# Optimization experiments

Measured on AMD Instinct MI355X. Metric: run time of the kernel, lower is better.

Reference implementation:

```python
import jax, jax.numpy as jnp
import numpy as np

B, T, D, H, FF = 4, 2048, 1024, 16, 4096
HD = D // H
EPS = 1e-5


def layernorm(x, g, b):
    m = jnp.mean(x, axis=-1, keepdims=True)
    v = jnp.var(x, axis=-1, keepdims=True)
    return (x - m) * jax.lax.rsqrt(v + EPS) * g + b


def setup_inputs() -> dict:
    key = jax.random.key(0)
    ks = jax.random.split(key, 12)
    s = lambda fan_in: 1.0 / np.sqrt(fan_in)
    x = jax.random.normal(ks[0], (B, T, D), dtype=jnp.float32)
    mask = jnp.tril(jnp.ones((T, T), dtype=jnp.int32))[None, None]  # [1,1,T,T] causal
    return {
        "x": x,
        "mask": mask,
        "ln1_g": jnp.ones((D,), jnp.float32),
        "ln1_b": jnp.zeros((D,), jnp.float32),
        "ln2_g": jnp.ones((D,), jnp.float32),
        "ln2_b": jnp.zeros((D,), jnp.float32),
        "qkv_w": jax.random.normal(ks[1], (D, 3 * D), jnp.float32) * s(D),
        "out_w": jax.random.normal(ks[2], (D, D), jnp.float32) * s(D),
        "out_b": jnp.zeros((D,), jnp.float32),
        "fc1_w": jax.random.normal(ks[3], (D, FF), jnp.float32) * s(D),
        "fc1_b": jnp.zeros((FF,), jnp.float32),
        "fc2_w": jax.random.normal(ks[4], (FF, D), jnp.float32) * s(FF),
        "fc2_b": jnp.zeros((D,), jnp.float32),
    }


def reference(x, mask, ln1_g, ln1_b, ln2_g, ln2_b, qkv_w, out_w, out_b,
              fc1_w, fc1_b, fc2_w, fc2_b):
    # --- attention sublayer (pre-LN) ---
    h = layernorm(x, ln1_g, ln1_b)
    qkv = h @ qkv_w  # [B,T,3D]
    q, k, v = jnp.split(qkv, 3, axis=-1)
    q = q.reshape(B, T, H, HD).transpose(0, 2, 1, 3)  # [B,H,T,hd]
    k = k.reshape(B, T, H, HD).transpose(0, 2, 1, 3)
    v = v.reshape(B, T, H, HD).transpose(0, 2, 1, 3)
    scale = 1.0 / np.sqrt(HD)
    scores = jnp.einsum('bhqd,bhkd->bhqk', q, k) * scale  # [B,H,T,T]
    scores = jnp.where(mask == 0, -jnp.inf, scores)
    attn = jax.nn.softmax(scores, axis=-1)
    o = jnp.einsum('bhqk,bhkd->bhqd', attn, v)
    o = o.transpose(0, 2, 1, 3).reshape(B, T, D)
    x = x + (o @ out_w + out_b)
    # --- MLP sublayer (pre-LN) ---
    h = layernorm(x, ln2_g, ln2_b)
    h = jax.nn.gelu(h @ fc1_w + fc1_b, approximate=False)
    x = x + (h @ fc2_w + fc2_b)
    return x
```

## Files before the change

### kernel.cpp

```cpp
#include <hip/hip_runtime.h>

typedef unsigned short bfraw;
typedef __attribute__((ext_vector_type(8))) short short8;
typedef __attribute__((ext_vector_type(4))) float f32x4;

__device__ __forceinline__ float b2f(bfraw u){ return __uint_as_float(((unsigned int)u)<<16); }
__device__ __forceinline__ bfraw f2b(float f){
  unsigned int u = __float_as_uint(f);
  return (bfraw)((u + 0x7FFFu + ((u>>16)&1u)) >> 16);
}
__device__ __forceinline__ void store_out(float* p, float v){ *p = v; }
__device__ __forceinline__ void store_out(bfraw* p, float v){ *p = f2b(v); }
__device__ __forceinline__ void gload_lds16(const bfraw* g, short* l) {
  __builtin_amdgcn_global_load_lds((const __attribute__((address_space(1))) void*)g,
                                   (__attribute__((address_space(3))) void*)l, 16, 0, 0);
}
__device__ __forceinline__ unsigned int cvt_pk_bf16(float a, float b) {
  unsigned int r;
  asm("v_cvt_pk_bf16_f32 %0, %1, %2" : "=v"(r) : "v"(a), "v"(b));
  return r;
}
__device__ __forceinline__ void waitvm3(){ asm volatile("s_waitcnt vmcnt(3)" ::: "memory"); }
__device__ __forceinline__ void waitvm0(){ asm volatile("s_waitcnt vmcnt(0)" ::: "memory"); }

__global__ __launch_bounds__(1024) void transpose_f32_bf16(const float* __restrict__ in,
                                                           bfraw* __restrict__ out,
                                                           int R, int C) {
  __shared__ bfraw tile[64][65];
  const int tx = threadIdx.x, ty = threadIdx.y;
  const int c0 = blockIdx.x*64, r0 = blockIdx.y*64;
  #pragma unroll
  for (int u = 0; u < 4; ++u)
    tile[ty + u*16][tx] = f2b(in[(size_t)(r0 + ty + u*16)*C + c0 + tx]);
  __syncthreads();
  #pragma unroll
  for (int u = 0; u < 4; ++u)
    out[(size_t)(c0 + ty + u*16)*R + r0 + tx] = tile[tx][ty + u*16];
}

__global__ __launch_bounds__(256) void ln_kernel(const float* __restrict__ x,
                                                 const float* __restrict__ g,
                                                 const float* __restrict__ b,
                                                 bfraw* __restrict__ out) {
  const int row = blockIdx.x, tid = threadIdx.x;
  const f32x4 v = ((const f32x4*)(x + (size_t)row*1024))[tid];
  float s  = v[0]+v[1]+v[2]+v[3];
  float s2 = v[0]*v[0]+v[1]*v[1]+v[2]*v[2]+v[3]*v[3];
  #pragma unroll
  for (int off = 1; off < 64; off <<= 1) { s += __shfl_xor(s, off); s2 += __shfl_xor(s2, off); }
  __shared__ float red[8];
  const int wv = tid>>6, ln_ = tid&63;
  if (ln_ == 0) { red[wv] = s; red[4+wv] = s2; }
  __syncthreads();
  float a  = red[0]+red[1]+red[2]+red[3];
  float a2 = red[4]+red[5]+red[6]+red[7];
  float mean = a*(1.0f/1024.0f);
  float var  = a2*(1.0f/1024.0f) - mean*mean;
  float inv  = rsqrtf(var + 1e-5f);
  const f32x4 gr = ((const f32x4*)g)[tid];
  const f32x4 br = ((const f32x4*)b)[tid];
  ushort4 o4;
  o4.x = f2b((v[0]-mean)*inv*gr[0] + br[0]);
  o4.y = f2b((v[1]-mean)*inv*gr[1] + br[1]);
  o4.z = f2b((v[2]-mean)*inv*gr[2] + br[2]);
  o4.w = f2b((v[3]-mean)*inv*gr[3] + br[3]);
  ((ushort4*)(out + (size_t)row*1024))[tid] = o4;
}

template<int EPI, typename OutT>
__global__ __launch_bounds__(512, 2) void gemm_bn128(const bfraw* __restrict__ A,
                                                     const bfraw* __restrict__ Bt,
                                                     const float* __restrict__ bias,
                                                     const float* __restrict__ resid,
                                                     OutT* __restrict__ C,
                                                     int M, int N, int K) {
  __shared__ __align__(16) short As[2*2*8192];
  __shared__ __align__(16) short Bs[2*2*4096];
  const int tid = threadIdx.x;
  const int wv = tid>>6, lane = tid&63;
  const int wm = wv>>1, wn = wv&1;
  const int q_ = lane>>4, r = lane&15;
  const int nbm = M>>8, nbn = N>>7;
  const int nwg = nbm*nbn;
  int id = (int)blockIdx.x;
  id = (id&7)*(nwg>>3) + (id>>3);
  const int bm = id % nbm, bn = id / nbm;

  const int srow = tid>>2, sch = tid&3;
  const int sP   = (srow&3) ^ ((srow>>2)&1);
  const int se   = ((sch ^ sP) << 3);
  const bfraw* Ag = A  + (size_t)(bm*256 + srow)*K + se;
  const bfraw* Bg = Bt + (size_t)(bn*128 + srow)*K + se;
  const size_t rowstepA = (size_t)128*K;

  auto stage = [&](int s, int k0s, int nb) {
    const bfraw* ga = Ag + k0s + s*32;
    short* da = As + (nb*2+s)*8192 + tid*8;
    gload_lds16(ga, da);
    gload_lds16(ga + rowstepA, da + 4096);
    const bfraw* gb = Bg + k0s + s*32;
    short* db = Bs + (nb*2+s)*4096 + tid*8;
    gload_lds16(gb, db);
  };

  const int xsw = ((q_ ^ (r&3) ^ ((r>>2)&1)) << 3);
  const int axo = (wm*64 + r)*32 + xsw;
  const int bxo = (wn*64 + r)*32 + xsw;

  f32x4 acc[4][4];
  #pragma unroll
  for (int mi = 0; mi < 4; ++mi)
    #pragma unroll
    for (int ni = 0; ni < 4; ++ni)
      acc[mi][ni] = (f32x4){0.f, 0.f, 0.f, 0.f};

  stage(0, 0, 0); stage(1, 0, 0);
  waitvm3();
  __builtin_amdgcn_s_barrier();

  const int ntiles = K >> 6;
  short8 af[4], bf[4];
  for (int t = 0; t < ntiles; ++t) {
    const int buf = t & 1, nb = buf ^ 1;
    const int k1 = (t + 1) << 6;
    const bool more = (t + 1) < ntiles;

    {
      const short* Ab = As + (buf*2+0)*8192;
      const short* Bb = Bs + (buf*2+0)*4096;
      #pragma unroll
      for (int ni = 0; ni < 4; ++ni) bf[ni] = *(const short8*)&Bb[bxo + ni*512];
      #pragma unroll
      for (int m = 0; m < 4; ++m)   af[m]  = *(const short8*)&Ab[axo + m*512];
    }
    if (more) stage(0, k1, nb);
    if (more) waitvm3(); else waitvm0();
    __builtin_amdgcn_s_barrier();
    __builtin_amdgcn_s_setprio(1);
    #pragma unroll
    for (int m = 0; m < 4; ++m)
      #pragma unroll
      for (int ni = 0; ni < 4; ++ni)
        acc[m][ni] = __builtin_amdgcn_mfma_f32_16x16x32_bf16(af[m], bf[ni], acc[m][ni], 0, 0, 0);
    __builtin_amdgcn_s_setprio(0);
    __builtin_amdgcn_s_barrier();

    {
      const short* Ab = As + (buf*2+1)*8192;
      const short* Bb = Bs + (buf*2+1)*4096;
      #pragma unroll
      for (int ni = 0; ni < 4; ++ni) bf[ni] = *(const short8*)&Bb[bxo + ni*512];
      #pragma unroll
      for (int m = 0; m < 4; ++m)   af[m]  = *(const short8*)&Ab[axo + m*512];
    }
    if (more) { stage(1, k1, nb); waitvm3(); }
    __builtin_amdgcn_s_barrier();
    __builtin_amdgcn_s_setprio(1);
    #pragma unroll
    for (int m = 0; m < 4; ++m)
      #pragma unroll
      for (int ni = 0; ni < 4; ++ni)
        acc[m][ni] = __builtin_amdgcn_mfma_f32_16x16x32_bf16(af[m], bf[ni], acc[m][ni], 0, 0, 0);
    __builtin_amdgcn_s_setprio(0);
    __builtin_amdgcn_s_barrier();
  }

  #pragma unroll
  for (int mi = 0; mi < 4; ++mi) {
    #pragma unroll
    for (int ni = 0; ni < 4; ++ni) {
      const int gcol = bn*128 + wn*64 + ni*16 + r;
      float bv = 0.f;
      if constexpr (EPI != 0) bv = bias[gcol];
      #pragma unroll
      for (int rg = 0; rg < 4; ++rg) {
        const int grow = bm*256 + wm*64 + mi*16 + q_*4 + rg;
        float val = acc[mi][ni][rg];
        if constexpr (EPI != 0) val += bv;
        if constexpr (EPI == 2) val = 0.5f*val*(1.0f + erff(val*0.70710678118654752f));
        if constexpr (EPI == 1) val += resid[(size_t)grow*N + gcol];
        store_out(&C[(size_t)grow*N + gcol], val);
      }
    }
  }
}

__global__ __launch_bounds__(256) void flash_attn(const bfraw* __restrict__ qkv,
                                                  bfraw* __restrict__ o) {
  __shared__ __align__(16) short Ksh[4096];
  __shared__ __align__(16) short Vts[4096];
  __shared__ __align__(16) short Psh[4096];
  const int tid = threadIdx.x;
  const int w = tid >> 6, lane = tid & 63;
  const int r = lane & 15, qd = lane >> 4;
  const int bb = blockIdx.y >> 4, h = blockIdx.y & 15;
  const size_t hb = (size_t)bb * 2048;
  short* Pw = &Psh[w * 1024];
  const int f0 = tid, f1 = tid + 256;
  const int key0 = f0 >> 3, dc0 = (f0 & 7) * 8;
  const int key1 = f1 >> 3, dc1 = (f1 & 7) * 8;

  for (int pass = 0; pass < 2; ++pass) {
    const int qt = pass ? (31 - (int)blockIdx.x) : (int)blockIdx.x;
    const int q0 = qt * 64;
    const int ntile = qt + 1;

    short8 qf[2];
    {
      const bfraw* qrow = qkv + (hb + q0 + w*16 + r) * 3072 + h*64;
      qf[0] = *(const short8*)(qrow + qd*8);
      qf[1] = *(const short8*)(qrow + qd*8 + 32);
    }

    f32x4 oacc[4];
    #pragma unroll
    for (int nt = 0; nt < 4; ++nt) oacc[nt] = (f32x4){0.f,0.f,0.f,0.f};
    float m_i = -3.0e38f;
    float l_i = 0.f;

    short8 kpre[2], vpre[2];
    {
      const bfraw* b0 = qkv + (hb + key0) * 3072 + h*64 + dc0;
      const bfraw* b1 = qkv + (hb + key1) * 3072 + h*64 + dc1;
      kpre[0] = *(const short8*)(b0 + 1024); vpre[0] = *(const short8*)(b0 + 2048);
      kpre[1] = *(const short8*)(b1 + 1024); vpre[1] = *(const short8*)(b1 + 2048);
    }

    for (int t = 0; t < ntile; ++t) {
      __syncthreads();
      #pragma unroll
      for (int pz = 0; pz < 2; ++pz) {
        const int key = pz ? key1 : key0, dc = pz ? dc1 : dc0;
        *(short8*)&Ksh[key*64 + ((((dc>>3) ^ (key>>3)) & 7) << 3)] = kpre[pz];
        const int kg = key >> 3, k7 = key & 7, dg = dc >> 3;
        #pragma unroll
        for (int i2 = 0; i2 < 8; ++i2)
          Vts[(dc + i2)*64 + (((kg ^ dg) & 7) << 3) + k7] = vpre[pz][i2];
      }
      __syncthreads();
      if (t + 1 < ntile) {
        const int j0n = (t + 1) * 64;
        const bfraw* b0 = qkv + (hb + j0n + key0) * 3072 + h*64 + dc0;
        const bfraw* b1 = qkv + (hb + j0n + key1) * 3072 + h*64 + dc1;
        kpre[0] = *(const short8*)(b0 + 1024); vpre[0] = *(const short8*)(b0 + 2048);
        kpre[1] = *(const short8*)(b1 + 1024); vpre[1] = *(const short8*)(b1 + 2048);
      }

      f32x4 s4[4];
      __builtin_amdgcn_s_setprio(1);
      #pragma unroll
      for (int kt = 0; kt < 4; ++kt) {
        f32x4 a = (f32x4){0.f,0.f,0.f,0.f};
        const int key = kt*16 + r, kgk = key >> 3;
        #pragma unroll
        for (int ks = 0; ks < 2; ++ks) {
          short8 kf8 = *(const short8*)&Ksh[key*64 + ((((qd + ks*4) ^ kgk) & 7) << 3)];
          a = __builtin_amdgcn_mfma_f32_16x16x32_bf16(kf8, qf[ks], a, 0, 0, 0);
        }
        s4[kt] = a;
      }
      __builtin_amdgcn_s_setprio(0);

      const bool diag = (t == qt);
      #pragma unroll
      for (int kt = 0; kt < 4; ++kt)
        #pragma unroll
        for (int rg = 0; rg < 4; ++rg) {
          float v = s4[kt][rg] * 0.125f;
          if (diag && (kt*16 + qd*4 + rg > w*16 + r)) v = -3.0e38f;
          s4[kt][rg] = v;
        }

      float mx = s4[0][0];
      #pragma unroll
      for (int kt = 0; kt < 4; ++kt)
        #pragma unroll
        for (int rg = 0; rg < 4; ++rg) mx = fmaxf(mx, s4[kt][rg]);
      mx = fmaxf(mx, __shfl_xor(mx, 16));
      mx = fmaxf(mx, __shfl_xor(mx, 32));
      const float mn = fmaxf(m_i, mx);
      const float alpha = __expf(m_i - mn);
      m_i = mn;
      l_i *= alpha;

      float lsum = 0.f;
      #pragma unroll
      for (int kt = 0; kt < 4; ++kt) {
        const float p0 = __expf(s4[kt][0] - mn);
        const float p1 = __expf(s4[kt][1] - mn);
        const float p2 = __expf(s4[kt][2] - mn);
        const float p3 = __expf(s4[kt][3] - mn);
        lsum += (p0 + p1) + (p2 + p3);
        uint2 pk;
        pk.x = cvt_pk_bf16(p0, p1);
        pk.y = cvt_pk_bf16(p2, p3);
        *(uint2*)((char*)Pw + r*128 + ((((kt*2 + (qd>>1)) ^ (r&7)) & 7) << 4) + ((qd&1)<<3)) = pk;
      }
      lsum += __shfl_xor(lsum, 16);
      lsum += __shfl_xor(lsum, 32);
      l_i += lsum;
      #pragma unroll
      for (int nt = 0; nt < 4; ++nt)
        #pragma unroll
        for (int rg = 0; rg < 4; ++rg) oacc[nt][rg] *= alpha;

      short8 pf[2];
      #pragma unroll
      for (int ks = 0; ks < 2; ++ks)
        pf[ks] = *(const short8*)&Pw[r*64 + ((((qd + ks*4) ^ (r & 7)) & 7) << 3)];
      __builtin_amdgcn_s_setprio(1);
      #pragma unroll
      for (int nt = 0; nt < 4; ++nt) {
        const int d = nt*16 + r, dg = d >> 3;
        #pragma unroll
        for (int ks = 0; ks < 2; ++ks) {
          short8 vf = *(const short8*)&Vts[d*64 + ((((qd + ks*4) ^ dg) & 7) << 3)];
          oacc[nt] = __builtin_amdgcn_mfma_f32_16x16x32_bf16(vf, pf[ks], oacc[nt], 0, 0, 0);
        }
      }
      __builtin_amdgcn_s_setprio(0);
    }

    const float invl = 1.0f / l_i;
    bfraw* orow = o + (hb + q0 + w*16 + r) * 1024 + h*64;
    #pragma unroll
    for (int nt = 0; nt < 4; ++nt) {
      uint2 ov;
      ov.x = cvt_pk_bf16(oacc[nt][0]*invl, oacc[nt][1]*invl);
      ov.y = cvt_pk_bf16(oacc[nt][2]*invl, oacc[nt][3]*invl);
      *(uint2*)(orow + nt*16 + qd*4) = ov;
    }
  }
}

extern "C" void kernel_launch(void* const* d_in, const int* in_sizes, int n_in,
                              void* d_out, int out_size, void* d_ws, size_t ws_size,
                              hipStream_t stream) {
  (void)in_sizes; (void)n_in;
  const float* x    = (const float*)d_in[0];
  const float* ln1g = (const float*)d_in[2];
  const float* ln1b = (const float*)d_in[3];
  const float* ln2g = (const float*)d_in[4];
  const float* ln2b = (const float*)d_in[5];
  const float* qkvw = (const float*)d_in[6];
  const float* outw = (const float*)d_in[7];
  const float* outb = (const float*)d_in[8];
  const float* fc1w = (const float*)d_in[9];
  const float* fc1b = (const float*)d_in[10];
  const float* fc2w = (const float*)d_in[11];
  const float* fc2b = (const float*)d_in[12];
  float* out = (float*)d_out;

  char* ws = (char*)d_ws;
  size_t off = 0;
  auto alloc = [&](size_t bytes) -> void* { void* p = ws + off; off += (bytes + 255) & ~(size_t)255; return p; };
  bfraw* wt_qkv = (bfraw*)alloc(3072ULL*1024*2);
  bfraw* wt_out = (bfraw*)alloc(1024ULL*1024*2);
  bfraw* wt_fc1 = (bfraw*)alloc(4096ULL*1024*2);
  bfraw* wt_fc2 = (bfraw*)alloc(1024ULL*4096*2);
  bfraw* hbuf   = (bfraw*)alloc(8192ULL*1024*2);
  float* x1     = (float*)alloc(8192ULL*1024*4);
  char*  big    = (char*) alloc(8192ULL*3072*2 + 8192ULL*1024*2);
  bfraw* qkv  = (bfraw*)big;
  bfraw* obuf = (bfraw*)(big + 8192ULL*3072*2);
  bfraw* hf   = (bfraw*)big;

  if (off > ws_size) {
    (void)hipMemsetAsync(d_out, 0x7F, (size_t)out_size*4, stream);
    return;
  }

  dim3 tb(64, 16);
  transpose_f32_bf16<<<dim3(48, 16), tb, 0, stream>>>(qkvw, wt_qkv, 1024, 3072);
  transpose_f32_bf16<<<dim3(16, 16), tb, 0, stream>>>(outw, wt_out, 1024, 1024);
  transpose_f32_bf16<<<dim3(64, 16), tb, 0, stream>>>(fc1w, wt_fc1, 1024, 4096);
  transpose_f32_bf16<<<dim3(16, 64), tb, 0, stream>>>(fc2w, wt_fc2, 4096, 1024);

  ln_kernel<<<8192, 256, 0, stream>>>(x, ln1g, ln1b, hbuf);
  gemm_bn128<0, bfraw><<<dim3(768), 512, 0, stream>>>(hbuf, wt_qkv, nullptr, nullptr, qkv, 8192, 3072, 1024);
  flash_attn<<<dim3(16, 64), 256, 0, stream>>>(qkv, obuf);
  gemm_bn128<1, float><<<dim3(256), 512, 0, stream>>>(obuf, wt_out, outb, x, x1, 8192, 1024, 1024);
  ln_kernel<<<8192, 256, 0, stream>>>(x1, ln2g, ln2b, hbuf);
  gemm_bn128<2, bfraw><<<dim3(1024), 512, 0, stream>>>(hbuf, wt_fc1, fc1b, nullptr, hf, 8192, 4096, 1024);
  gemm_bn128<1, float><<<dim3(256), 512, 0, stream>>>(hf, wt_fc2, fc2b, x1, out, 8192, 1024, 4096);
}
```

Before: 616.8 us.

## Rewrite GEMM as 8-phase pipelined kernel with BN=256 tile for FC1

Replaces the GEMM main loop with a finer-grained schedule of four MFMA phases per K-tile. Each phase interleaves LDS fragment loads with global-to-LDS staging of half-slabs two tiles ahead, and waits on explicit vmcnt/lgkmcnt counts. The LDS layout uses a new 8-way XOR swizzle with 64-element rows, and the kernel is templated on BN so FC1 can use a 256-wide tile with a 2x4 warp layout. The goal is to hide global load latency and LDS bank conflicts behind MFMA work and to raise reuse for the largest GEMM. The cost is more register pressure, more barriers, and hand-tuned wait counts that could be fragile.

```diff
diff --git a/kernel.cpp b/kernel.cpp
--- a/kernel.cpp
+++ b/kernel.cpp
@@ -20,8 +20,6 @@
   asm("v_cvt_pk_bf16_f32 %0, %1, %2" : "=v"(r) : "v"(a), "v"(b));
   return r;
 }
-__device__ __forceinline__ void waitvm3(){ asm volatile("s_waitcnt vmcnt(3)" ::: "memory"); }
-__device__ __forceinline__ void waitvm0(){ asm volatile("s_waitcnt vmcnt(0)" ::: "memory"); }
 
 __global__ __launch_bounds__(1024) void transpose_f32_bf16(const float* __restrict__ in,
                                                            bfraw* __restrict__ out,
@@ -67,114 +65,191 @@
   ((ushort4*)(out + (size_t)row*1024))[tid] = o4;
 }
 
-template<int EPI, typename OutT>
-__global__ __launch_bounds__(512, 2) void gemm_bn128(const bfraw* __restrict__ A,
-                                                     const bfraw* __restrict__ Bt,
-                                                     const float* __restrict__ bias,
-                                                     const float* __restrict__ resid,
-                                                     OutT* __restrict__ C,
-                                                     int M, int N, int K) {
+template<int BN, int EPI, typename OutT>
+__global__ __launch_bounds__(512, 2) void gemm8p(const bfraw* __restrict__ A,
+                                                 const bfraw* __restrict__ Bt,
+                                                 const float* __restrict__ bias,
+                                                 const float* __restrict__ resid,
+                                                 OutT* __restrict__ C,
+                                                 int M, int N, int K) {
+  constexpr int WM  = (BN==256)?2:4;
+  constexpr int WN  = 8/WM;
+  constexpr int MR  = (256/WM)/16;
+  constexpr int MRH = MR/2;
+  constexpr int RPA = 16*MRH;
+  constexpr int LB  = BN/128;
+  constexpr int SLABB = BN*32;
   __shared__ __align__(16) short As[2*2*8192];
-  __shared__ __align__(16) short Bs[2*2*4096];
+  __shared__ __align__(16) short Bs[2*2*SLABB];
   const int tid = threadIdx.x;
   const int wv = tid>>6, lane = tid&63;
-  const int wm = wv>>1, wn = wv&1;
-  const int q_ = lane>>4, r = lane&15;
-  const int nbm = M>>8, nbn = N>>7;
+  const int wm = wv / WN, wn = wv % WN;
+  const int q_ = lane>>4, r = lane&15, r7 = r&7;
+
+  const int nbm = M>>8, nbn = N/BN;
   const int nwg = nbm*nbn;
   int id = (int)blockIdx.x;
   id = (id&7)*(nwg>>3) + (id>>3);
   const int bm = id % nbm, bn = id / nbm;
 
-  const int srow = tid>>2, sch = tid&3;
-  const int sP   = (srow&3) ^ ((srow>>2)&1);
-  const int se   = ((sch ^ sP) << 3);
-  const bfraw* Ag = A  + (size_t)(bm*256 + srow)*K + se;
-  const bfraw* Bg = Bt + (size_t)(bn*128 + srow)*K + se;
-  const size_t rowstepA = (size_t)128*K;
-
-  auto stage = [&](int s, int k0s, int nb) {
-    const bfraw* ga = Ag + k0s + s*32;
-    short* da = As + (nb*2+s)*8192 + tid*8;
-    gload_lds16(ga, da);
-    gload_lds16(ga + rowstepA, da + 4096);
-    const bfraw* gb = Bg + k0s + s*32;
-    short* db = Bs + (nb*2+s)*4096 + tid*8;
-    gload_lds16(gb, db);
+  const int i0 = tid>>3;
+  const int chs = (tid&7) ^ (i0&7);
+  unsigned int aoff[2][2], boff[LB][2];
+  #pragma unroll
+  for (int l = 0; l < 2; ++l)
+    #pragma unroll
+    for (int s = 0; s < 2; ++s) {
+      const int i = l*64 + i0;
+      const int g = (i/RPA)*(256/WM) + s*RPA + (i%RPA);
+      aoff[l][s] = (unsigned int)(bm*256 + g)*(unsigned int)K + chs*8;
+    }
+  #pragma unroll
+  for (int l = 0; l < LB; ++l)
+    #pragma unroll
+    for (int s = 0; s < 2; ++s) {
+      const int i = l*64 + i0;
+      const int g = (i>>5)*64 + s*32 + (i&31);
+      boff[l][s] = (unsigned int)(bn*BN + g)*(unsigned int)K + chs*8;
+    }
+  auto stA = [&](int s, int kb, int b) {
+    #pragma unroll
+    for (int l = 0; l < 2; ++l)
+      gload_lds16(A + aoff[l][s] + kb, As + (b*2+s)*8192 + (l*512+tid)*8);
   };
-
-  const int xsw = ((q_ ^ (r&3) ^ ((r>>2)&1)) << 3);
-  const int axo = (wm*64 + r)*32 + xsw;
-  const int bxo = (wn*64 + r)*32 + xsw;
-
-  f32x4 acc[4][4];
-  #pragma unroll
-  for (int mi = 0; mi < 4; ++mi)
+  auto stB = [&](int s, int kb, int b) {
+    #pragma unroll
+    for (int l = 0; l < LB; ++l)
+      gload_lds16(Bt + boff[l][s] + kb, Bs + (b*2+s)*SLABB + (l*512+tid)*8);
+  };
+
+  const int afb = (wm*RPA + r)*64;
+  const int bfb = (wn*32  + r)*64;
+  const int csw0 = ((q_     ^ r7) << 3);
+  const int csw1 = (((4+q_) ^ r7) << 3);
+
+  f32x4 acc[MR][4];
+  #pragma unroll
+  for (int mi = 0; mi < MR; ++mi)
     #pragma unroll
     for (int ni = 0; ni < 4; ++ni)
       acc[mi][ni] = (f32x4){0.f, 0.f, 0.f, 0.f};
 
-  stage(0, 0, 0); stage(1, 0, 0);
-  waitvm3();
+  stA(0,0,0); stB(0,0,0); stA(1,0,0); stB(1,0,0);
+  stA(0,64,1); stB(0,64,1); stA(1,64,1);
+  if constexpr (BN==256) asm volatile("s_waitcnt vmcnt(6)" ::: "memory");
+  else                   asm volatile("s_waitcnt vmcnt(5)" ::: "memory");
   __builtin_amdgcn_s_barrier();
 
-  const int ntiles = K >> 6;
-  short8 af[4], bf[4];
-  for (int t = 0; t < ntiles; ++t) {
-    const int buf = t & 1, nb = buf ^ 1;
-    const int k1 = (t + 1) << 6;
-    const bool more = (t + 1) < ntiles;
+  const int nt = K >> 6;
+  short8 af0[2][MRH], af1[2][MRH], bf0[2][2], bf1[2][2];
+  for (int t = 0; t < nt; ++t) {
+    const int buf = t & 1, ob = buf ^ 1;
+    const int k1 = (t + 1) << 6, k2 = (t + 2) << 6;
+    const bool m1 = (t + 1) < nt, m2 = (t + 2) < nt;
 
     {
       const short* Ab = As + (buf*2+0)*8192;
-      const short* Bb = Bs + (buf*2+0)*4096;
-      #pragma unroll
-      for (int ni = 0; ni < 4; ++ni) bf[ni] = *(const short8*)&Bb[bxo + ni*512];
-      #pragma unroll
-      for (int m = 0; m < 4; ++m)   af[m]  = *(const short8*)&Ab[axo + m*512];
-    }
-    if (more) stage(0, k1, nb);
-    if (more) waitvm3(); else waitvm0();
-    __builtin_amdgcn_s_barrier();
+      const short* Bb = Bs + (buf*2+0)*SLABB;
+      #pragma unroll
+      for (int n = 0; n < 2; ++n) {
+        bf0[0][n] = *(const short8*)&Bb[bfb + n*1024 + csw0];
+        bf0[1][n] = *(const short8*)&Bb[bfb + n*1024 + csw1];
+      }
+      #pragma unroll
+      for (int m = 0; m < MRH; ++m) {
+        af0[0][m] = *(const short8*)&Ab[afb + m*1024 + csw0];
+        af0[1][m] = *(const short8*)&Ab[afb + m*1024 + csw1];
+      }
+    }
+    if (m1) stB(1, k1, ob);
+    if constexpr (BN==256) asm volatile("s_waitcnt lgkmcnt(8)" ::: "memory");
+    __builtin_amdgcn_s_barrier();
+    asm volatile("s_waitcnt lgkmcnt(0)" ::: "memory");
     __builtin_amdgcn_s_setprio(1);
     #pragma unroll
-    for (int m = 0; m < 4; ++m)
-      #pragma unroll
-      for (int ni = 0; ni < 4; ++ni)
-        acc[m][ni] = __builtin_amdgcn_mfma_f32_16x16x32_bf16(af[m], bf[ni], acc[m][ni], 0, 0, 0);
+    for (int m = 0; m < MRH; ++m)
+      #pragma unroll
+      for (int n = 0; n < 2; ++n) {
+        acc[m][n] = __builtin_amdgcn_mfma_f32_16x16x32_bf16(af0[0][m], bf0[0][n], acc[m][n], 0, 0, 0);
+        acc[m][n] = __builtin_amdgcn_mfma_f32_16x16x32_bf16(af0[1][m], bf0[1][n], acc[m][n], 0, 0, 0);
+      }
     __builtin_amdgcn_s_setprio(0);
     __builtin_amdgcn_s_barrier();
 
     {
       const short* Ab = As + (buf*2+1)*8192;
-      const short* Bb = Bs + (buf*2+1)*4096;
-      #pragma unroll
-      for (int ni = 0; ni < 4; ++ni) bf[ni] = *(const short8*)&Bb[bxo + ni*512];
-      #pragma unroll
-      for (int m = 0; m < 4; ++m)   af[m]  = *(const short8*)&Ab[axo + m*512];
-    }
-    if (more) { stage(1, k1, nb); waitvm3(); }
-    __builtin_amdgcn_s_barrier();
+      #pragma unroll
+      for (int m = 0; m < MRH; ++m) {
+        af1[0][m] = *(const short8*)&Ab[afb + m*1024 + csw0];
+        af1[1][m] = *(const short8*)&Ab[afb + m*1024 + csw1];
+      }
+    }
+    if (m2) stA(0, k2, buf);
+    __builtin_amdgcn_s_barrier();
+    asm volatile("s_waitcnt lgkmcnt(0)" ::: "memory");
     __builtin_amdgcn_s_setprio(1);
     #pragma unroll
-    for (int m = 0; m < 4; ++m)
-      #pragma unroll
-      for (int ni = 0; ni < 4; ++ni)
-        acc[m][ni] = __builtin_amdgcn_mfma_f32_16x16x32_bf16(af[m], bf[ni], acc[m][ni], 0, 0, 0);
+    for (int m = 0; m < MRH; ++m)
+      #pragma unroll
+      for (int n = 0; n < 2; ++n) {
+        acc[MRH+m][n] = __builtin_amdgcn_mfma_f32_16x16x32_bf16(af1[0][m], bf0[0][n], acc[MRH+m][n], 0, 0, 0);
+        acc[MRH+m][n] = __builtin_amdgcn_mfma_f32_16x16x32_bf16(af1[1][m], bf0[1][n], acc[MRH+m][n], 0, 0, 0);
+      }
     __builtin_amdgcn_s_setprio(0);
     __builtin_amdgcn_s_barrier();
+
+    {
+      const short* Bb = Bs + (buf*2+1)*SLABB;
+      #pragma unroll
+      for (int n = 0; n < 2; ++n) {
+        bf1[0][n] = *(const short8*)&Bb[bfb + n*1024 + csw0];
+        bf1[1][n] = *(const short8*)&Bb[bfb + n*1024 + csw1];
+      }
+    }
+    if (m2) stB(0, k2, buf);
+    __builtin_amdgcn_s_barrier();
+    asm volatile("s_waitcnt lgkmcnt(0)" ::: "memory");
+    __builtin_amdgcn_s_setprio(1);
+    #pragma unroll
+    for (int m = 0; m < MRH; ++m)
+      #pragma unroll
+      for (int n = 0; n < 2; ++n) {
+        acc[m][2+n] = __builtin_amdgcn_mfma_f32_16x16x32_bf16(af0[0][m], bf1[0][n], acc[m][2+n], 0, 0, 0);
+        acc[m][2+n] = __builtin_amdgcn_mfma_f32_16x16x32_bf16(af0[1][m], bf1[1][n], acc[m][2+n], 0, 0, 0);
+      }
+    __builtin_amdgcn_s_setprio(0);
+    __builtin_amdgcn_s_barrier();
+
+    if (m2) stA(1, k2, buf);
+    if (m2) {
+      if constexpr (BN==256) asm volatile("s_waitcnt vmcnt(6)" ::: "memory");
+      else                   asm volatile("s_waitcnt vmcnt(5)" ::: "memory");
+    } else if (m1) {
+      asm volatile("s_waitcnt vmcnt(0)" ::: "memory");
+    }
+    __builtin_amdgcn_s_barrier();
+    __builtin_amdgcn_s_setprio(1);
+    #pragma unroll
+    for (int m = 0; m < MRH; ++m)
+      #pragma unroll
+      for (int n = 0; n < 2; ++n) {
+        acc[MRH+m][2+n] = __builtin_amdgcn_mfma_f32_16x16x32_bf16(af1[0][m], bf1[0][n], acc[MRH+m][2+n], 0, 0, 0);
+        acc[MRH+m][2+n] = __builtin_amdgcn_mfma_f32_16x16x32_bf16(af1[1][m], bf1[1][n], acc[MRH+m][2+n], 0, 0, 0);
+      }
+    __builtin_amdgcn_s_setprio(0);
+    __builtin_amdgcn_s_barrier();
   }
 
   #pragma unroll
-  for (int mi = 0; mi < 4; ++mi) {
+  for (int mi = 0; mi < MR; ++mi) {
     #pragma unroll
     for (int ni = 0; ni < 4; ++ni) {
-      const int gcol = bn*128 + wn*64 + ni*16 + r;
+      const int gcol = bn*BN + wn*64 + ni*16 + r;
       float bv = 0.f;
       if constexpr (EPI != 0) bv = bias[gcol];
       #pragma unroll
       for (int rg = 0; rg < 4; ++rg) {
-        const int grow = bm*256 + wm*64 + mi*16 + q_*4 + rg;
+        const int grow = bm*256 + wm*(MR*16) + mi*16 + q_*4 + rg;
         float val = acc[mi][ni][rg];
         if constexpr (EPI != 0) val += bv;
         if constexpr (EPI == 2) val = 0.5f*val*(1.0f + erff(val*0.70710678118654752f));
@@ -377,10 +452,10 @@
   transpose_f32_bf16<<<dim3(16, 64), tb, 0, stream>>>(fc2w, wt_fc2, 4096, 1024);
 
   ln_kernel<<<8192, 256, 0, stream>>>(x, ln1g, ln1b, hbuf);
-  gemm_bn128<0, bfraw><<<dim3(768), 512, 0, stream>>>(hbuf, wt_qkv, nullptr, nullptr, qkv, 8192, 3072, 1024);
+  gemm8p<128, 0, bfraw><<<dim3(768), 512, 0, stream>>>(hbuf, wt_qkv, nullptr, nullptr, qkv, 8192, 3072, 1024);
   flash_attn<<<dim3(16, 64), 256, 0, stream>>>(qkv, obuf);
-  gemm_bn128<1, float><<<dim3(256), 512, 0, stream>>>(obuf, wt_out, outb, x, x1, 8192, 1024, 1024);
+  gemm8p<128, 1, float><<<dim3(256), 512, 0, stream>>>(obuf, wt_out, outb, x, x1, 8192, 1024, 1024);
   ln_kernel<<<8192, 256, 0, stream>>>(x1, ln2g, ln2b, hbuf);
-  gemm_bn128<2, bfraw><<<dim3(1024), 512, 0, stream>>>(hbuf, wt_fc1, fc1b, nullptr, hf, 8192, 4096, 1024);
-  gemm_bn128<1, float><<<dim3(256), 512, 0, stream>>>(hf, wt_fc2, fc2b, x1, out, 8192, 1024, 4096);
-}
+  gemm8p<256, 2, bfraw><<<dim3(512), 512, 0, stream>>>(hbuf, wt_fc1, fc1b, nullptr, hf, 8192, 4096, 1024);
+  gemm8p<128, 1, float><<<dim3(256), 512, 0, stream>>>(hf, wt_fc2, fc2b, x1, out, 8192, 1024, 4096);
+}
```

After: 607.2 us. Within noise of the previous version (-1.6%).
